# Performance work log

Measured on AMD Instinct MI355X. Metric: run time of the kernel, lower is better.

Reference implementation:

```python
import jax, jax.numpy as jnp
import numpy as np

N = 50000      # n_nodes
E = 800000     # n_edges
D = 64         # in_dim == out_dim
K = 3          # k-neighbourhoods {1,2,3} at t=2
T = 2          # layer index t
NU = 1         # cfg.nu -> delay(k) = max(k - nu, 0)
AGG_EPS = 1e-6
BN_EPS = 1e-5


def setup_inputs() -> dict:
    key = jax.random.key(0)
    ks = jax.random.split(key, 8)
    xs = jax.random.normal(ks[0], (T + 1, N, D), dtype=jnp.float32)
    edge_index = jax.random.randint(ks[1], (2, E), 0, N, dtype=jnp.int32)
    edge_attr = jax.random.randint(ks[2], (E,), 1, K + 1, dtype=jnp.int32)  # hop k in {1..K}
    s = 1.0 / np.sqrt(D)
    Wa = jax.random.normal(ks[3], (D, D), dtype=jnp.float32) * s
    Wd = jax.random.normal(ks[4], (D, D), dtype=jnp.float32) * s
    Wb = jax.random.normal(ks[5], (K, D, D), dtype=jnp.float32) * s
    return {
        "xs": xs,
        "edge_index": edge_index,
        "edge_attr": edge_attr,
        "Wa": Wa, "ba": jnp.zeros((D,), jnp.float32),
        "Wd": Wd, "bd": jnp.zeros((D,), jnp.float32),
        "Wb": Wb, "bb": jnp.zeros((K, D), jnp.float32),
        "gamma": jnp.ones((D,), jnp.float32),
        "beta": jnp.zeros((D,), jnp.float32),
    }


def reference(xs, edge_index, edge_attr, Wa, ba, Wd, bd, Wb, bb, gamma, beta):
    # current node state
    x = xs[T]  # [N, D]
    # delayed state per hop k: xs[t - max(k - nu, 0)] -> indices [2, 1, 0] for k = 1,2,3
    state_idx = jnp.array([T - max(k - NU, 0) for k in range(1, K + 1)])
    states = xs[state_idx]                                   # [K, N, D]
    # per-k linear B_k (source uses B for both Bx and Ex)
    Bx = jnp.einsum('knd,kdo->kno', states, Wb) + bb[:, None, :]  # [K, N, D]
    Ex = Bx
    Ax = x @ Wa + ba                                         # [N, D]
    Dx = x @ Wd + bd                                         # [N, D]

    i_idx = edge_index[1]                                    # destination
    j_idx = edge_index[0]                                    # source
    ke = edge_attr - 1                                       # [E], 0..K-1

    Dx_i = Dx[i_idx]                                         # [E, D]
    Ex_j = Ex[ke, j_idx]                                     # [E, D] per-k gather
    Bx_j = Bx[ke, j_idx]                                     # [E, D]

    sigma = jax.nn.sigmoid(Dx_i + Ex_j)                      # [E, D]

    # per-(node, k) scatter-sum; segment id packs (i, k)
    seg = i_idx * K + ke
    num = jax.ops.segment_sum(sigma * Bx_j, seg, num_segments=N * K).reshape(N, K, D)
    den = jax.ops.segment_sum(sigma, seg, num_segments=N * K).reshape(N, K, D)
    eta = num / (den + AGG_EPS)                              # [N, K, D]

    alpha = 1.0 / K  # softmax(ones(K)) with convex combination
    x_new = Ax + alpha * eta.sum(axis=1)                     # [N, D]

    # BatchNorm1d over nodes (training-mode batch statistics, biased var)
    mean = x_new.mean(axis=0)
    var = jnp.var(x_new, axis=0)
    y = gamma * (x_new - mean) * jax.lax.rsqrt(var + BN_EPS) + beta
    return jax.nn.relu(y)  # dropout p=0.0, residual=False
```

## Files before the change

### kernel.cpp

```cpp
#include <hip/hip_runtime.h>
#include <hip/hip_bf16.h>

#define D 64
#define K 3

typedef __hip_bfloat16 bf16;

__device__ __forceinline__ float b2f(bf16 v) { return __bfloat162float(v); }

#define P_WA 0
#define P_BA 4096
#define P_WD 4160
#define P_BD 8256
#define P_WB 8320
#define P_BB 20608
#define P_G  20800
#define P_B  20864
#define P_TOTAL 20928

#define LOG2E 1.442695041f

__global__ void cvt_count_kernel(const void* Wa, const void* ba, const void* Wd, const void* bd,
                                 const void* Wb, const void* bb, const void* g, const void* b,
                                 float* __restrict__ P, int* __restrict__ flag,
                                 const int* __restrict__ ei, const int* __restrict__ ea,
                                 int* __restrict__ cnt, int E, int eblocks, int cb)
{
    const int bid = blockIdx.x;
    if (bid < eblocks) {
        const int e = bid * 256 + threadIdx.x;
        if (e < E) {
            const int i  = ei[E + e];
            const int ke = ea[e] - 1;
            atomicAdd(&cnt[i * K + ke], 1);
        }
        return;
    }
    const int isbf = (((const unsigned int*)g)[0] == 0x3F803F80u) ? 1 : 0;
    if (bid == eblocks && threadIdx.x == 0) *flag = isbf;
    int i = (bid - eblocks) * 256 + threadIdx.x;
    const int stride = cb * 256;
    for (; i < P_TOTAL; i += stride) {
        const void* src; int off;
        if (i < P_BA)      { src = Wa; off = i; }
        else if (i < P_WD) { src = ba; off = i - P_BA; }
        else if (i < P_BD) { src = Wd; off = i - P_WD; }
        else if (i < P_WB) { src = bd; off = i - P_BD; }
        else if (i < P_BB) { src = Wb; off = i - P_WB; }
        else if (i < P_G)  { src = bb; off = i - P_BB; }
        else if (i < P_B)  { src = g;  off = i - P_G; }
        else               { src = b;  off = i - P_B; }
        float v;
        if (isbf) v = b2f(((const bf16*)src)[off]);
        else      v = ((const float*)src)[off];
        P[i] = v;
    }
}

union U8 { float4 f; ushort4 u; };

__device__ __forceinline__ void lin_load(U8 reg[8], const void* xs_raw, size_t xbase,
                                         int isbf, int tid, int nbase, int N)
{
    if (isbf) {
        const ushort* xp = (const ushort*)xs_raw + xbase;
        #pragma unroll
        for (int p = 0; p < 8; p++) {
            const int idx = tid + (p << 8);
            const int n = nbase + (idx >> 4), c4 = (idx & 15) << 2;
            if (n < N) reg[p].u = *(const ushort4*)(xp + (size_t)n * D + c4);
            else       reg[p].u = make_ushort4(0, 0, 0, 0);
        }
    } else {
        const float* xp = (const float*)xs_raw + xbase;
        #pragma unroll
        for (int p = 0; p < 8; p++) {
            const int idx = tid + (p << 8);
            const int n = nbase + (idx >> 4), c4 = (idx & 15) << 2;
            if (n < N) reg[p].f = *(const float4*)(xp + (size_t)n * D + c4);
            else       reg[p].f = make_float4(0.f, 0.f, 0.f, 0.f);
        }
    }
}

__global__ void lin_scan_kernel(const void* __restrict__ xs_raw,
                                const float* __restrict__ P, const int* __restrict__ flag,
                                float* __restrict__ Ax, float* __restrict__ Dx,
                                float* __restrict__ Bx, int N,
                                int* __restrict__ cnt, int* __restrict__ btot,
                                int M, int gx, int LB)
{
    __shared__ __align__(16) float sw[64][64];
    __shared__ float sx[128][65];
    __shared__ float sbias[64];
    __shared__ int sscan[256];

    const int bid = blockIdx.x;
    const int tid = threadIdx.x;

    if (bid >= LB) {
        const int sb = bid - LB;
        const int base = sb * 1024 + tid * 4;
        int v[4];
        #pragma unroll
        for (int q = 0; q < 4; q++) {
            const int i = base + q;
            v[q] = (i < M) ? cnt[i] : 0;
        }
        const int tsum = v[0] + v[1] + v[2] + v[3];
        sscan[tid] = tsum;
        __syncthreads();
        #pragma unroll
        for (int o = 1; o < 256; o <<= 1) {
            int x = (tid >= o) ? sscan[tid - o] : 0;
            __syncthreads();
            sscan[tid] += x;
            __syncthreads();
        }
        int run = sscan[tid] - tsum;
        #pragma unroll
        for (int q = 0; q < 4; q++) {
            const int i = base + q;
            if (i < M) cnt[i] = run;
            run += v[q];
        }
        if (tid == 255) btot[sb] = sscan[tid];
        return;
    }

    const int which = bid / gx;
    const int t0    = bid % gx;

    const float* W; const float* bias; size_t xbase; float* out;
    if (which == 0)      { W = P + P_WA; bias = P + P_BA; xbase = (size_t)2 * N * D; out = Ax; }
    else if (which == 1) { W = P + P_WD; bias = P + P_BD; xbase = (size_t)2 * N * D; out = Dx; }
    else {
        const int k = which - 2;
        W = P + P_WB + (size_t)k * D * D;
        bias = P + P_BB + (size_t)k * D;
        const int layer = 2 - k;
        xbase = (size_t)layer * N * D;
        out = Bx + (size_t)k * N * D;
    }

    for (int idx = tid; idx < D * D; idx += 256)
        sw[idx >> 6][idx & 63] = W[idx];
    if (tid < 64) sbias[tid] = bias[tid];

    const int isbf = *flag;
    const int tiles = (N + 127) >> 7;

    U8 reg[8];
    int t = t0;
    if (t < tiles) lin_load(reg, xs_raw, xbase, isbf, tid, t << 7, N);

    const int ct = tid & 7;  const int c0 = ct * 8;
    const int nt = tid >> 3; const int n0 = nt * 4;

    for (; t < tiles; t += gx) {
        __syncthreads();
        #pragma unroll
        for (int p = 0; p < 8; p++) {
            const int idx = tid + (p << 8);
            const int n = idx >> 4, c4 = (idx & 15) << 2;
            float v0, v1, v2, v3;
            if (isbf) {
                v0 = __uint_as_float((unsigned)reg[p].u.x << 16);
                v1 = __uint_as_float((unsigned)reg[p].u.y << 16);
                v2 = __uint_as_float((unsigned)reg[p].u.z << 16);
                v3 = __uint_as_float((unsigned)reg[p].u.w << 16);
            } else {
                v0 = reg[p].f.x; v1 = reg[p].f.y; v2 = reg[p].f.z; v3 = reg[p].f.w;
            }
            sx[n][c4 + 0] = v0; sx[n][c4 + 1] = v1;
            sx[n][c4 + 2] = v2; sx[n][c4 + 3] = v3;
        }
        __syncthreads();

        const int tn = t + gx;
        if (tn < tiles) lin_load(reg, xs_raw, xbase, isbf, tid, tn << 7, N);

        float acc[4][8];
        {
            float b0[8];
            #pragma unroll
            for (int j = 0; j < 8; j++) b0[j] = sbias[c0 + j];
            #pragma unroll
            for (int i = 0; i < 4; i++)
                #pragma unroll
                for (int j = 0; j < 8; j++) acc[i][j] = b0[j];
        }

        #pragma unroll 8
        for (int kk = 0; kk < 64; kk++) {
            const float4 wlo = *(const float4*)&sw[kk][c0];
            const float4 whi = *(const float4*)&sw[kk][c0 + 4];
            float xv[4];
            #pragma unroll
            for (int i = 0; i < 4; i++) xv[i] = sx[n0 + i][kk];
            #pragma unroll
            for (int i = 0; i < 4; i++) {
                acc[i][0] += xv[i] * wlo.x; acc[i][1] += xv[i] * wlo.y;
                acc[i][2] += xv[i] * wlo.z; acc[i][3] += xv[i] * wlo.w;
                acc[i][4] += xv[i] * whi.x; acc[i][5] += xv[i] * whi.y;
                acc[i][6] += xv[i] * whi.z; acc[i][7] += xv[i] * whi.w;
            }
        }

        const int nbase = t << 7;
        #pragma unroll
        for (int i = 0; i < 4; i++) {
            const int gn = nbase + n0 + i;
            if (gn < N) {
                float* op = out + (size_t)gn * D + c0;
                *(float4*)op       = make_float4(acc[i][0], acc[i][1], acc[i][2], acc[i][3]);
                *(float4*)(op + 4) = make_float4(acc[i][4], acc[i][5], acc[i][6], acc[i][7]);
            }
        }
    }
}

__global__ void scan2_kernel(int* __restrict__ btot, int* __restrict__ boff, int nb)
{
    __shared__ int s[256];
    const int t = threadIdx.x;
    const int v = (t < nb) ? btot[t] : 0;
    s[t] = v;
    __syncthreads();
    #pragma unroll
    for (int o = 1; o < 256; o <<= 1) {
        int x = (t >= o) ? s[t - o] : 0;
        __syncthreads();
        s[t] += x;
        __syncthreads();
    }
    if (t < nb) boff[t] = s[t] - v;
}

__global__ void scatter_kernel(const int* __restrict__ ei, const int* __restrict__ ea,
                               const int* __restrict__ cnt, const int* __restrict__ boff,
                               int* __restrict__ cur, int* __restrict__ elist, int E)
{
    const int e = blockIdx.x * blockDim.x + threadIdx.x;
    if (e >= E) return;
    const int j  = ei[e];
    const int i  = ei[E + e];
    const int ke = ea[e] - 1;
    const int seg = i * K + ke;
    const int pos = atomicAdd(&cur[seg], 1);
    elist[cnt[seg] + boff[seg >> 10] + pos] = j;
}

__global__ void node_kernel(float* __restrict__ Ax,
                            const float* __restrict__ Dx, const float* __restrict__ Bx,
                            const int* __restrict__ cnt, const int* __restrict__ boff,
                            const int* __restrict__ elist,
                            float* __restrict__ statsP, int N, int E)
{
    __shared__ float red[256];
    const int tid = threadIdx.x;
    const int w = tid >> 6, d = tid & 63;
    const size_t ND = (size_t)N * D;
    const int M = N * K;

    float lsum = 0.f, lsq = 0.f;
    for (int n = blockIdx.x * 4 + w; n < N; n += gridDim.x * 4) {
        const float dx = Dx[(size_t)n * D + d];
        const float ndx = dx * -LOG2E;
        const int b0 = n * K;
        const int o0 = cnt[b0]     + boff[b0 >> 10];
        const int o1 = cnt[b0 + 1] + boff[(b0 + 1) >> 10];
        const int o2 = cnt[b0 + 2] + boff[(b0 + 2) >> 10];
        const int o3 = (b0 + 3 < M) ? cnt[b0 + 3] + boff[(b0 + 3) >> 10] : E;
        int wb = o0;
        int jv = (wb + d < o3) ? elist[wb + d] : 0;
        float eta = 0.f;
        #pragma unroll
        for (int k = 0; k < K; k++) {
            const float* __restrict__ bxk = Bx + (size_t)k * ND;
            const int sbeg = (k == 0) ? o0 : (k == 1) ? o1 : o2;
            const int send = (k == 0) ? o1 : (k == 1) ? o2 : o3;
            float num = 0.f, den = 0.f;
            int p = sbeg;
            while (p < send) {
                if (p - wb >= 64) {
                    wb = p;
                    jv = (wb + d < o3) ? elist[wb + d] : 0;
                }
                int lim = wb + 64; if (lim > send) lim = send;
                int c = p - wb;
                const int cend = lim - wb;
                for (; c + 3 < cend; c += 4) {
                    const int j0 = __builtin_amdgcn_readlane(jv, c);
                    const int j1 = __builtin_amdgcn_readlane(jv, c + 1);
                    const int j2 = __builtin_amdgcn_readlane(jv, c + 2);
                    const int j3 = __builtin_amdgcn_readlane(jv, c + 3);
                    const float bx0 = (bxk + ((size_t)(unsigned)j0 << 6))[d];
                    const float bx1 = (bxk + ((size_t)(unsigned)j1 << 6))[d];
                    const float bx2 = (bxk + ((size_t)(unsigned)j2 << 6))[d];
                    const float bx3 = (bxk + ((size_t)(unsigned)j3 << 6))[d];
                    const float s0 = __builtin_amdgcn_rcpf(1.f + __builtin_amdgcn_exp2f(fmaf(bx0, -LOG2E, ndx)));
                    const float s1 = __builtin_amdgcn_rcpf(1.f + __builtin_amdgcn_exp2f(fmaf(bx1, -LOG2E, ndx)));
                    const float s2 = __builtin_amdgcn_rcpf(1.f + __builtin_amdgcn_exp2f(fmaf(bx2, -LOG2E, ndx)));
                    const float s3 = __builtin_amdgcn_rcpf(1.f + __builtin_amdgcn_exp2f(fmaf(bx3, -LOG2E, ndx)));
                    num = fmaf(s0, bx0, num); den += s0;
                    num = fmaf(s1, bx1, num); den += s1;
                    num = fmaf(s2, bx2, num); den += s2;
                    num = fmaf(s3, bx3, num); den += s3;
                }
                for (; c < cend; ++c) {
                    const int j0 = __builtin_amdgcn_readlane(jv, c);
                    const float bx0 = (bxk + ((size_t)(unsigned)j0 << 6))[d];
                    const float s0 = __builtin_amdgcn_rcpf(1.f + __builtin_amdgcn_exp2f(fmaf(bx0, -LOG2E, ndx)));
                    num = fmaf(s0, bx0, num); den += s0;
                }
                p = lim;
            }
            eta = fmaf(num, __builtin_amdgcn_rcpf(den + 1e-6f), eta);
        }
        const size_t xi = (size_t)n * D + d;
        const float v = Ax[xi] + eta * (1.f / 3.f);
        Ax[xi] = v;
        lsum += v;
        lsq  += v * v;
    }

    red[tid] = lsum;
    __syncthreads();
    if (tid < 64) {
        float* sp = statsP + (size_t)(blockIdx.x & 63) * 128;
        atomicAdd(&sp[d], red[d] + red[64 + d] + red[128 + d] + red[192 + d]);
    }
    __syncthreads();
    red[tid] = lsq;
    __syncthreads();
    if (tid < 64) {
        float* sp = statsP + (size_t)(blockIdx.x & 63) * 128;
        atomicAdd(&sp[64 + d], red[d] + red[64 + d] + red[128 + d] + red[192 + d]);
    }
}

__global__ void bnreduce_kernel(const float* __restrict__ statsP, float* __restrict__ stats)
{
    const int t = threadIdx.x;
    float a = 0.f;
    for (int c = 0; c < 64; c++) a += statsP[c * 128 + t];
    stats[t] = a;
}

__global__ void finalize_kernel(const float* __restrict__ xnew, const float* __restrict__ stats,
                                const float* __restrict__ P, const int* __restrict__ flag,
                                void* __restrict__ out, int N)
{
    const long long g = (long long)blockIdx.x * blockDim.x + threadIdx.x;
    if (g >= (long long)N * D) return;
    const int d = (int)(g & 63);

    const float invN = 1.f / (float)N;
    const float mean = stats[d] * invN;
    const float var  = stats[64 + d] * invN - mean * mean;
    const float rstd = rsqrtf(var + 1e-5f);

    float y = P[P_G + d] * (xnew[g] - mean) * rstd + P[P_B + d];
    y = fmaxf(y, 0.f);

    if (*flag) ((bf16*)out)[g] = __float2bfloat16(y);
    else       ((float*)out)[g] = y;
}

extern "C" void kernel_launch(void* const* d_in, const int* in_sizes, int n_in,
                              void* d_out, int out_size, void* d_ws, size_t ws_size,
                              hipStream_t stream)
{
    const void* xs = d_in[0];
    const int*  ei = (const int*)d_in[1];
    const int*  ea = (const int*)d_in[2];

    const int N = in_sizes[0] / (3 * D);
    const int E = in_sizes[2];
    const int M = N * K;

    float* ws = (float*)d_ws;
    const size_t nd = (size_t)N * D;

    float* P      = ws;
    int*   flag   = (int*)(P + P_TOTAL);
    float* Ax     = (float*)(flag + 1);
    float* Dx     = Ax + nd;
    float* Bx     = Dx + nd;
    float* statsP = Bx + 3 * nd;
    float* stats  = statsP + 64 * 128;
    int*   cnt    = (int*)(stats + 128);
    int*   cur    = cnt + (M + 1);
    int*   btot   = cur + M;
    int*   boff   = btot + 256;
    int*   elist  = boff + 256;

    const size_t zbytes = (size_t)(64 * 128 + 128) * 4 + ((size_t)(M + 1) + M + 512) * 4;
    hipMemsetAsync(statsP, 0, zbytes, stream);

    const int eblocks = (E + 255) / 256;
    const int cb = 82;
    cvt_count_kernel<<<eblocks + cb, 256, 0, stream>>>(
        d_in[3], d_in[4], d_in[5], d_in[6], d_in[7], d_in[8], d_in[9], d_in[10],
        P, flag, ei, ea, cnt, E, eblocks, cb);

    const int tiles = (N + 127) / 128;
    const int gx = (tiles < 144) ? tiles : 144;
    const int LB = gx * 5;
    const int nsb = (M + 1023) / 1024;
    lin_scan_kernel<<<LB + nsb, 256, 0, stream>>>(xs, P, flag, Ax, Dx, Bx, N,
                                                  cnt, btot, M, gx, LB);

    scan2_kernel<<<1, 256, 0, stream>>>(btot, boff, nsb);

    scatter_kernel<<<eblocks, 256, 0, stream>>>(ei, ea, cnt, boff, cur, elist, E);

    node_kernel<<<2048, 256, 0, stream>>>(Ax, Dx, Bx, cnt, boff, elist, statsP, N, E);

    bnreduce_kernel<<<1, 128, 0, stream>>>(statsP, stats);

    finalize_kernel<<<(int)((nd + 255) / 256), 256, 0, stream>>>(Ax, stats, P, flag, d_out, N);
}
```

Before: 282.4 us.

## Replace global per-segment counting sort with two-level bucket sort of edges

Edge CSR construction moves from per-segment global atomics (count, two-level scan, scatter) to a two-level scheme. Edges are first histogrammed into buckets of 128 destination nodes using shared-memory atomics, then scattered into buckets as packed (local node, hop, source) words. A per-bucket kernel then sorts them locally and writes the segment offsets. This cuts global atomic contention, removes the scan2 kernel and the large zeroed count arrays, and gives node_kernel direct offsets. In exchange the edge list is read and written more times, and the packing assumes source index below 2^17 and NB ≤ 1024.

```diff
diff --git a/kernel.cpp b/kernel.cpp
--- a/kernel.cpp
+++ b/kernel.cpp
@@ -20,25 +20,37 @@
 
 #define LOG2E 1.442695041f
 
-__global__ void cvt_count_kernel(const void* Wa, const void* ba, const void* Wd, const void* bd,
-                                 const void* Wb, const void* bb, const void* g, const void* b,
-                                 float* __restrict__ P, int* __restrict__ flag,
-                                 const int* __restrict__ ei, const int* __restrict__ ea,
-                                 int* __restrict__ cnt, int E, int eblocks, int cb)
-{
+#define NB_MAX 1024
+#define BKN    128
+#define BKSEG  (BKN * K)
+
+__global__ void cvt_hist_kernel(const void* Wa, const void* ba, const void* Wd, const void* bd,
+                                const void* Wb, const void* bb, const void* g, const void* b,
+                                float* __restrict__ P, int* __restrict__ flag,
+                                const int* __restrict__ ei,
+                                int* __restrict__ bcnt, int E, int HB, int cb, int NB)
+{
+    __shared__ int bins[NB_MAX];
     const int bid = blockIdx.x;
-    if (bid < eblocks) {
-        const int e = bid * 256 + threadIdx.x;
-        if (e < E) {
-            const int i  = ei[E + e];
-            const int ke = ea[e] - 1;
-            atomicAdd(&cnt[i * K + ke], 1);
+    const int tid = threadIdx.x;
+
+    if (bid < HB) {
+        for (int i = tid; i < NB; i += 256) bins[i] = 0;
+        __syncthreads();
+        const int tstr = HB * 256;
+        for (int e = bid * 256 + tid; e < E; e += tstr)
+            atomicAdd(&bins[ei[E + e] >> 7], 1);
+        __syncthreads();
+        for (int i = tid; i < NB; i += 256) {
+            const int c = bins[i];
+            if (c) atomicAdd(&bcnt[i], c);
         }
         return;
     }
+
     const int isbf = (((const unsigned int*)g)[0] == 0x3F803F80u) ? 1 : 0;
-    if (bid == eblocks && threadIdx.x == 0) *flag = isbf;
-    int i = (bid - eblocks) * 256 + threadIdx.x;
+    if (bid == HB && tid == 0) *flag = isbf;
+    int i = (bid - HB) * 256 + tid;
     const int stride = cb * 256;
     for (; i < P_TOTAL; i += stride) {
         const void* src; int off;
@@ -87,8 +99,9 @@
                                 const float* __restrict__ P, const int* __restrict__ flag,
                                 float* __restrict__ Ax, float* __restrict__ Dx,
                                 float* __restrict__ Bx, int N,
-                                int* __restrict__ cnt, int* __restrict__ btot,
-                                int M, int gx, int LB)
+                                const int* __restrict__ bcnt, int* __restrict__ bbase,
+                                int* __restrict__ bcur, int* __restrict__ off,
+                                int M, int E, int NB, int gx, int LB)
 {
     __shared__ __align__(16) float sw[64][64];
     __shared__ float sx[128][65];
@@ -99,13 +112,12 @@
     const int tid = threadIdx.x;
 
     if (bid >= LB) {
-        const int sb = bid - LB;
-        const int base = sb * 1024 + tid * 4;
+        const int base = tid * 4;
         int v[4];
         #pragma unroll
         for (int q = 0; q < 4; q++) {
             const int i = base + q;
-            v[q] = (i < M) ? cnt[i] : 0;
+            v[q] = (i < NB) ? bcnt[i] : 0;
         }
         const int tsum = v[0] + v[1] + v[2] + v[3];
         sscan[tid] = tsum;
@@ -121,10 +133,10 @@
         #pragma unroll
         for (int q = 0; q < 4; q++) {
             const int i = base + q;
-            if (i < M) cnt[i] = run;
+            if (i < NB) { bbase[i] = run; bcur[i] = run; }
             run += v[q];
         }
-        if (tid == 255) btot[sb] = sscan[tid];
+        if (tid == 0) off[M] = E;
         return;
     }
 
@@ -220,58 +232,99 @@
     }
 }
 
-__global__ void scan2_kernel(int* __restrict__ btot, int* __restrict__ boff, int nb)
-{
-    __shared__ int s[256];
-    const int t = threadIdx.x;
-    const int v = (t < nb) ? btot[t] : 0;
-    s[t] = v;
-    __syncthreads();
-    #pragma unroll
-    for (int o = 1; o < 256; o <<= 1) {
-        int x = (t >= o) ? s[t - o] : 0;
-        __syncthreads();
-        s[t] += x;
-        __syncthreads();
-    }
-    if (t < nb) boff[t] = s[t] - v;
-}
-
-__global__ void scatter_kernel(const int* __restrict__ ei, const int* __restrict__ ea,
-                               const int* __restrict__ cnt, const int* __restrict__ boff,
-                               int* __restrict__ cur, int* __restrict__ elist, int E)
-{
-    const int e = blockIdx.x * blockDim.x + threadIdx.x;
-    if (e >= E) return;
-    const int j  = ei[e];
-    const int i  = ei[E + e];
-    const int ke = ea[e] - 1;
-    const int seg = i * K + ke;
-    const int pos = atomicAdd(&cur[seg], 1);
-    elist[cnt[seg] + boff[seg >> 10] + pos] = j;
+__global__ void binscat_kernel(const int* __restrict__ ei, const int* __restrict__ ea,
+                               int* __restrict__ bcur, int* __restrict__ bkt,
+                               int E, int NB, int CH)
+{
+    __shared__ int lcnt[NB_MAX];
+    __shared__ int lbase[NB_MAX];
+    const int bid = blockIdx.x, tid = threadIdx.x;
+    const int s0 = bid * CH;
+    int s1 = s0 + CH; if (s1 > E) s1 = E;
+
+    for (int i = tid; i < NB; i += 256) lcnt[i] = 0;
+    __syncthreads();
+    for (int e = s0 + tid; e < s1; e += 256)
+        atomicAdd(&lcnt[ei[E + e] >> 7], 1);
+    __syncthreads();
+    for (int b = tid; b < NB; b += 256) {
+        const int c = lcnt[b];
+        lbase[b] = c ? atomicAdd(&bcur[b], c) : 0;
+        lcnt[b] = 0;
+    }
+    __syncthreads();
+    for (int e = s0 + tid; e < s1; e += 256) {
+        const int i  = ei[E + e];
+        const int j  = ei[e];
+        const int ke = ea[e] - 1;
+        const int b  = i >> 7;
+        const int r  = atomicAdd(&lcnt[b], 1);
+        bkt[lbase[b] + r] = ((i & 127) << 19) | (ke << 17) | j;
+    }
+}
+
+__global__ void bucketsort_kernel(const int* __restrict__ bbase, const int* __restrict__ bcur,
+                                  const int* __restrict__ bkt,
+                                  int* __restrict__ off, int* __restrict__ elist, int M)
+{
+    __shared__ int cl[512];
+    __shared__ int cu[512];
+    const int b = blockIdx.x, tid = threadIdx.x;
+    const int s0 = bbase[b], s1 = bcur[b];
+
+    cl[tid] = 0; cl[tid + 256] = 0;
+    __syncthreads();
+    for (int idx = s0 + tid; idx < s1; idx += 256) {
+        const int p = bkt[idx];
+        atomicAdd(&cl[(p >> 19) * 3 + ((p >> 17) & 3)], 1);
+    }
+    __syncthreads();
+    const int c0 = cl[tid], c1 = cl[tid + 256];
+    for (int o = 1; o < 512; o <<= 1) {
+        const int a0 = (tid >= o) ? cl[tid - o] : 0;
+        const int a1 = cl[tid + 256 - o];
+        __syncthreads();
+        cl[tid] += a0; cl[tid + 256] += a1;
+        __syncthreads();
+    }
+    const int e0 = cl[tid] - c0, e1 = cl[tid + 256] - c1;
+    cu[tid] = e0; cu[tid + 256] = e1;
+    const int gbase = b * BKSEG;
+    {
+        const int gs0 = gbase + tid;
+        if (tid < BKSEG && gs0 < M) off[gs0] = s0 + e0;
+        const int ls1 = tid + 256;
+        const int gs1 = gbase + ls1;
+        if (ls1 < BKSEG && gs1 < M) off[gs1] = s0 + e1;
+    }
+    __syncthreads();
+    for (int idx = s0 + tid; idx < s1; idx += 256) {
+        const int p = bkt[idx];
+        const int ls = (p >> 19) * 3 + ((p >> 17) & 3);
+        const int pos = atomicAdd(&cu[ls], 1);
+        elist[s0 + pos] = p & 0x1FFFF;
+    }
 }
 
 __global__ void node_kernel(float* __restrict__ Ax,
                             const float* __restrict__ Dx, const float* __restrict__ Bx,
-                            const int* __restrict__ cnt, const int* __restrict__ boff,
-                            const int* __restrict__ elist,
-                            float* __restrict__ statsP, int N, int E)
+                            const int* __restrict__ off, const int* __restrict__ elist,
+                            float* __restrict__ statsP, int N)
 {
     __shared__ float red[256];
     const int tid = threadIdx.x;
     const int w = tid >> 6, d = tid & 63;
     const size_t ND = (size_t)N * D;
-    const int M = N * K;
 
     float lsum = 0.f, lsq = 0.f;
     for (int n = blockIdx.x * 4 + w; n < N; n += gridDim.x * 4) {
         const float dx = Dx[(size_t)n * D + d];
         const float ndx = dx * -LOG2E;
-        const int b0 = n * K;
-        const int o0 = cnt[b0]     + boff[b0 >> 10];
-        const int o1 = cnt[b0 + 1] + boff[(b0 + 1) >> 10];
-        const int o2 = cnt[b0 + 2] + boff[(b0 + 2) >> 10];
-        const int o3 = (b0 + 3 < M) ? cnt[b0 + 3] + boff[(b0 + 3) >> 10] : E;
+        const int b0 = n * 3;
+        const int o0 = off[b0];
+        const int o1 = off[b0 + 1];
+        const int o2 = off[b0 + 2];
+        const int o3 = off[b0 + 3];
         int wb = o0;
         int jv = (wb + d < o3) ? elist[wb + d] : 0;
         float eta = 0.f;
@@ -379,6 +432,7 @@
     const int N = in_sizes[0] / (3 * D);
     const int E = in_sizes[2];
     const int M = N * K;
+    const int NB = (N + BKN - 1) / BKN;
 
     float* ws = (float*)d_ws;
     const size_t nd = (size_t)N * D;
@@ -390,33 +444,35 @@
     float* Bx     = Dx + nd;
     float* statsP = Bx + 3 * nd;
     float* stats  = statsP + 64 * 128;
-    int*   cnt    = (int*)(stats + 128);
-    int*   cur    = cnt + (M + 1);
-    int*   btot   = cur + M;
-    int*   boff   = btot + 256;
-    int*   elist  = boff + 256;
-
-    const size_t zbytes = (size_t)(64 * 128 + 128) * 4 + ((size_t)(M + 1) + M + 512) * 4;
+    int*   bcnt   = (int*)(stats + 128);
+    int*   bbase  = bcnt + NB_MAX;
+    int*   bcur   = bbase + NB_MAX;
+    int*   off    = bcur + NB_MAX;
+    int*   bkt    = off + (M + 1);
+    int*   elist  = bkt + E;
+
+    const size_t zbytes = (size_t)(64 * 128 + 128 + NB_MAX) * 4;
     hipMemsetAsync(statsP, 0, zbytes, stream);
 
-    const int eblocks = (E + 255) / 256;
+    const int HB = 128;
     const int cb = 82;
-    cvt_count_kernel<<<eblocks + cb, 256, 0, stream>>>(
+    cvt_hist_kernel<<<HB + cb, 256, 0, stream>>>(
         d_in[3], d_in[4], d_in[5], d_in[6], d_in[7], d_in[8], d_in[9], d_in[10],
-        P, flag, ei, ea, cnt, E, eblocks, cb);
+        P, flag, ei, bcnt, E, HB, cb, NB);
 
     const int tiles = (N + 127) / 128;
     const int gx = (tiles < 144) ? tiles : 144;
     const int LB = gx * 5;
-    const int nsb = (M + 1023) / 1024;
-    lin_scan_kernel<<<LB + nsb, 256, 0, stream>>>(xs, P, flag, Ax, Dx, Bx, N,
-                                                  cnt, btot, M, gx, LB);
-
-    scan2_kernel<<<1, 256, 0, stream>>>(btot, boff, nsb);
-
-    scatter_kernel<<<eblocks, 256, 0, stream>>>(ei, ea, cnt, boff, cur, elist, E);
-
-    node_kernel<<<2048, 256, 0, stream>>>(Ax, Dx, Bx, cnt, boff, elist, statsP, N, E);
+    lin_scan_kernel<<<LB + 1, 256, 0, stream>>>(xs, P, flag, Ax, Dx, Bx, N,
+                                                bcnt, bbase, bcur, off, M, E, NB, gx, LB);
+
+    const int HB2 = 128;
+    const int CH = (E + HB2 - 1) / HB2;
+    binscat_kernel<<<HB2, 256, 0, stream>>>(ei, ea, bcur, bkt, E, NB, CH);
+
+    bucketsort_kernel<<<NB, 256, 0, stream>>>(bbase, bcur, bkt, off, elist, M);
+
+    node_kernel<<<2048, 256, 0, stream>>>(Ax, Dx, Bx, off, elist, statsP, N);
 
     bnreduce_kernel<<<1, 128, 0, stream>>>(statsP, stats);
 
```

Measured after the change: 241.0 us. 14.7% less time.
